# Performance work log

Hardware: AMD Instinct MI355X
Metric: run time of the kernel (lower is better)

The kernel has to match this reference:

```python
import jax, jax.numpy as jnp
import numpy as np

EPS = 1e-8  # torch.cosine_similarity norm clamp

def setup_inputs() -> dict:
    key = jax.random.key(0)
    k1, k2, k3, k4 = jax.random.split(key, 4)
    B, S, D, C = 64, 512, 768, 512
    V = jax.random.normal(k1, (B, S, D), dtype=jnp.float32)
    label_embeddings = jax.random.normal(k2, (C, D), dtype=jnp.float32)
    fc_w = jax.random.normal(k3, (C, D), dtype=jnp.float32) * 0.02
    fc_b = jax.random.normal(k4, (C,), dtype=jnp.float32) * 0.02
    return {"V": V, "label_embeddings": label_embeddings, "fc_w": fc_w, "fc_b": fc_b}

def reference(V, label_embeddings, fc_w, fc_b):
    # Normalized embeddings (cosine similarity = dot of unit vectors, norms clamped at EPS)
    Vn = V / jnp.maximum(jnp.linalg.norm(V, axis=-1, keepdims=True), EPS)
    Ln = label_embeddings / jnp.maximum(
        jnp.linalg.norm(label_embeddings, axis=-1, keepdims=True), EPS)
    # [B, S, C] cosine similarities, then max over classes -> per-token weight m [B, S]
    sims = jnp.einsum('bsd,cd->bsc', Vn, Ln)
    m = jnp.max(sims, axis=-1)
    # Softmax over sequence dim -> attention beta [B, S]
    beta = jax.nn.softmax(m, axis=-1)
    # Weighted sum of token embeddings: z = V^T beta  -> [B, D]
    z = jnp.einsum('bsd,bs->bd', V, beta)
    # Final classifier
    out = z @ fc_w.T + fc_b
    return (out, z)
```

## Files before the change

kernel.cpp:

```cpp
#include <hip/hip_runtime.h>
#include <cstdint>
#include <cstddef>

#define BB 64
#define SS 512
#define DD 768
#define CC 512

typedef __attribute__((ext_vector_type(8))) short short8;
typedef __attribute__((ext_vector_type(4))) float f32x4;

#define GLOBAL_AS __attribute__((address_space(1)))
#define LDS_AS __attribute__((address_space(3)))

static __device__ __forceinline__ unsigned short f2bf(float f) {
  union { float f; unsigned u; } v; v.f = f;
  unsigned u = v.u;
  u += 0x7FFFu + ((u >> 16) & 1u);
  return (unsigned short)(u >> 16);
}

static __device__ __forceinline__ void async_copy16(const void* g, void* l) {
  __builtin_amdgcn_global_load_lds((const GLOBAL_AS void*)g, (LDS_AS void*)l,
                                   16, 0, 0);
}

__global__ __launch_bounds__(256) void k_label_norm(const float* __restrict__ L,
                                                    unsigned short* __restrict__ Lnb) {
  const int c = blockIdx.x;
  const int tid = threadIdx.x;
  const float* row = L + (size_t)c * DD;
  float v[3];
  float s = 0.f;
#pragma unroll
  for (int k = 0; k < 3; k++) { v[k] = row[tid + 256 * k]; s += v[k] * v[k]; }
#pragma unroll
  for (int o = 32; o > 0; o >>= 1) s += __shfl_xor(s, o, 64);
  __shared__ float wsum[4];
  if ((tid & 63) == 0) wsum[tid >> 6] = s;
  __syncthreads();
  const float tot = wsum[0] + wsum[1] + wsum[2] + wsum[3];
  const float inv = 1.f / fmaxf(sqrtf(tot), 1e-8f);
  unsigned short* orow = Lnb + (size_t)c * DD;
  const int sw = c & 7;
#pragma unroll
  for (int k = 0; k < 3; k++) {
    const int d = tid + 256 * k;
    const int idx = (((d >> 3) ^ sw) << 3) | (d & 7);
    orow[idx] = f2bf(v[k] * inv);
  }
}

__global__ __launch_bounds__(256) void k_sims_max(const float* __restrict__ V,
                                                  const unsigned short* __restrict__ Lnb,
                                                  float* __restrict__ m_out) {
  const int tid = threadIdx.x;
  const int wave = tid >> 6;
  const int lane = tid & 63;
  const int q = lane >> 4;
  const int mr = lane & 15;
  const int64_t tokBase = (int64_t)blockIdx.x * 64 + wave * 16;

  __shared__ unsigned short Bs[2][16 * DD];
  __shared__ float nrmS[4][16];

  {
    const char* src = (const char*)(Lnb + (size_t)0 * 16 * DD);
    char* dst = (char*)&Bs[0][0];
#pragma unroll
    for (int i = wave; i < 24; i += 4)
      async_copy16(src + i * 1024 + lane * 16, dst + i * 1024);
  }

  const float* arow = V + (tokBase + mr) * DD + q * 8;
  short8 afrag[24];
  float nrm2 = 0.f;
#pragma unroll
  for (int kc = 0; kc < 24; kc++) {
    const float4* p = (const float4*)(arow + kc * 32);
    const float4 x = p[0];
    const float4 y = p[1];
    short8 a;
    a[0] = (short)f2bf(x.x); a[1] = (short)f2bf(x.y);
    a[2] = (short)f2bf(x.z); a[3] = (short)f2bf(x.w);
    a[4] = (short)f2bf(y.x); a[5] = (short)f2bf(y.y);
    a[6] = (short)f2bf(y.z); a[7] = (short)f2bf(y.w);
    afrag[kc] = a;
    nrm2 += x.x * x.x + x.y * x.y + x.z * x.z + x.w * x.w;
    nrm2 += y.x * y.x + y.y * y.y + y.z * y.z + y.w * y.w;
  }
  nrm2 += __shfl_xor(nrm2, 16, 64);
  nrm2 += __shfl_xor(nrm2, 32, 64);
  if (q == 0) nrmS[wave][mr] = nrm2;

  __syncthreads();

  const int sw = mr & 7;
  f32x4 vmax = {-3e38f, -3e38f, -3e38f, -3e38f};
  for (int cc = 0; cc < 32; cc++) {
    const int p = cc & 1;
    if (cc + 1 < 32) {
      const char* src = (const char*)(Lnb + (size_t)(cc + 1) * 16 * DD);
      char* dst = (char*)&Bs[p ^ 1][0];
#pragma unroll
      for (int i = wave; i < 24; i += 4)
        async_copy16(src + i * 1024 + lane * 16, dst + i * 1024);
    }
    f32x4 acc = {0.f, 0.f, 0.f, 0.f};
#pragma unroll
    for (int kc = 0; kc < 24; kc++) {
      const int off = mr * DD + (((kc << 2) + q) ^ sw) * 8;
      const short8 b = *(const short8*)&Bs[p][off];
      acc = __builtin_amdgcn_mfma_f32_16x16x32_bf16(afrag[kc], b, acc, 0, 0, 0);
    }
    vmax[0] = fmaxf(vmax[0], acc[0]);
    vmax[1] = fmaxf(vmax[1], acc[1]);
    vmax[2] = fmaxf(vmax[2], acc[2]);
    vmax[3] = fmaxf(vmax[3], acc[3]);
    __syncthreads();
  }
#pragma unroll
  for (int o = 1; o < 16; o <<= 1) {
#pragma unroll
    for (int r = 0; r < 4; r++) vmax[r] = fmaxf(vmax[r], __shfl_xor(vmax[r], o, 64));
  }
  if (mr == 0) {
#pragma unroll
    for (int r = 0; r < 4; r++) {
      const float nr = nrmS[wave][q * 4 + r];
      m_out[tokBase + q * 4 + r] = vmax[r] / fmaxf(sqrtf(nr), 1e-8f);
    }
  }
}

__global__ __launch_bounds__(256) void k_softmax(const float* __restrict__ m,
                                                 float* __restrict__ beta) {
  const int b = blockIdx.x;
  const int tid = threadIdx.x;
  const float* mb = m + (size_t)b * SS;
  const float v0 = mb[tid];
  const float v1 = mb[tid + 256];
  float mx = fmaxf(v0, v1);
#pragma unroll
  for (int o = 32; o > 0; o >>= 1) mx = fmaxf(mx, __shfl_xor(mx, o, 64));
  __shared__ float wred[4];
  if ((tid & 63) == 0) wred[tid >> 6] = mx;
  __syncthreads();
  mx = fmaxf(fmaxf(wred[0], wred[1]), fmaxf(wred[2], wred[3]));
  const float e0 = __expf(v0 - mx);
  const float e1 = __expf(v1 - mx);
  float s = e0 + e1;
#pragma unroll
  for (int o = 32; o > 0; o >>= 1) s += __shfl_xor(s, o, 64);
  __syncthreads();
  if ((tid & 63) == 0) wred[tid >> 6] = s;
  __syncthreads();
  s = wred[0] + wred[1] + wred[2] + wred[3];
  const float inv = 1.f / s;
  float* bb = beta + (size_t)b * SS;
  bb[tid] = e0 * inv;
  bb[tid + 256] = e1 * inv;
}

__global__ __launch_bounds__(192) void k_zpart(const float* __restrict__ V,
                                               const float* __restrict__ beta,
                                               float* __restrict__ zpart,
                                               int spc, int nsc) {
  const int blk = blockIdx.x;
  const int b = blk / nsc;
  const int sc = blk % nsc;
  const int tid = threadIdx.x;
  const float* vb = V + ((size_t)b * SS + (size_t)sc * spc) * DD + tid * 4;
  const float* bb = beta + (size_t)b * SS + (size_t)sc * spc;
  float4 acc = {0.f, 0.f, 0.f, 0.f};
#pragma unroll 4
  for (int s = 0; s < spc; s++) {
    const float w = bb[s];
    const float4 x = *(const float4*)(vb + (size_t)s * DD);
    acc.x += w * x.x; acc.y += w * x.y; acc.z += w * x.z; acc.w += w * x.w;
  }
  *(float4*)(zpart + (size_t)blk * DD + tid * 4) = acc;
}

__global__ __launch_bounds__(256) void k_final(const float* __restrict__ zpart,
                                               const float* __restrict__ fc_w,
                                               const float* __restrict__ fc_b,
                                               float* __restrict__ out,
                                               float* __restrict__ zout,
                                               int nsc) {
  const int b = blockIdx.x >> 1;
  const int half = blockIdx.x & 1;
  const int tid = threadIdx.x;
  __shared__ float zs[DD];
  for (int i = tid; i < DD; i += 256) {
    float s = 0.f;
    for (int sc = 0; sc < nsc; sc++) s += zpart[((size_t)b * nsc + sc) * DD + i];
    zs[i] = s;
    if (half == 0) zout[(size_t)b * DD + i] = s;
  }
  __syncthreads();
  const int c = half * 256 + tid;
  const float4* w = (const float4*)(fc_w + (size_t)c * DD);
  float acc = 0.f;
  for (int d4 = 0; d4 < DD / 4; d4++) {
    const float4 ww = w[d4];
    acc += ww.x * zs[d4 * 4] + ww.y * zs[d4 * 4 + 1] +
           ww.z * zs[d4 * 4 + 2] + ww.w * zs[d4 * 4 + 3];
  }
  out[(size_t)b * CC + c] = acc + fc_b[c];
}

extern "C" void kernel_launch(void* const* d_in, const int* in_sizes, int n_in,
                              void* d_out, int out_size, void* d_ws, size_t ws_size,
                              hipStream_t stream) {
  const float* V  = (const float*)d_in[0];
  const float* L  = (const float*)d_in[1];
  const float* fw = (const float*)d_in[2];
  const float* fb = (const float*)d_in[3];
  float* out = (float*)d_out;

  char* ws = (char*)d_ws;
  unsigned short* Lnb = (unsigned short*)ws;
  float* m     = (float*)(ws + 786432);
  float* beta  = (float*)(ws + 917504);
  float* zpart = (float*)(ws + 1048576);

  const int nsc = (ws_size >= (size_t)1048576 + 16 * BB * DD * 4) ? 16 : 8;
  const int spc = SS / nsc;

  k_label_norm<<<CC, 256, 0, stream>>>(L, Lnb);
  k_sims_max<<<512, 256, 0, stream>>>(V, Lnb, m);
  k_softmax<<<BB, 256, 0, stream>>>(m, beta);
  k_zpart<<<BB * nsc, 192, 0, stream>>>(V, beta, zpart, spc, nsc);
  k_final<<<2 * BB, 256, 0, stream>>>(zpart, fw, fb, out, out + BB * CC, nsc);
}
```

Before: 242.5 us.

## Double tokens per wave in sims kernel and fuse softmax into z partials

The sims-max kernel now runs two waves per block, each handling 32 tokens, so every LDS B-fragment load feeds two MFMAs. Each token tile also spreads its MFMAs across four independent accumulators to break the dependency chain. The separate softmax kernel is removed: each k_zpart block recomputes the row max and exp-sum from m and applies exp weights inline, saving a launch and the beta round trip at the cost of redundant reduction work per block. Register pressure rises (48 A fragments), and fewer waves per block may reduce latency hiding.

After: 259.6 us. +7.1%, slower.

```diff
diff --git a/kernel.cpp b/kernel.cpp
--- a/kernel.cpp
+++ b/kernel.cpp
@@ -51,134 +51,155 @@
   }
 }
 
-__global__ __launch_bounds__(256) void k_sims_max(const float* __restrict__ V,
-                                                  const unsigned short* __restrict__ Lnb,
-                                                  float* __restrict__ m_out) {
+__global__ __launch_bounds__(128, 1) void k_sims_max(const float* __restrict__ V,
+                                                     const unsigned short* __restrict__ Lnb,
+                                                     float* __restrict__ m_out) {
   const int tid = threadIdx.x;
   const int wave = tid >> 6;
   const int lane = tid & 63;
   const int q = lane >> 4;
   const int mr = lane & 15;
-  const int64_t tokBase = (int64_t)blockIdx.x * 64 + wave * 16;
+  const int64_t tokBase = (int64_t)blockIdx.x * 64 + wave * 32;
 
   __shared__ unsigned short Bs[2][16 * DD];
-  __shared__ float nrmS[4][16];
+  __shared__ float nrmS[2][32];
 
   {
-    const char* src = (const char*)(Lnb + (size_t)0 * 16 * DD);
+    const char* src = (const char*)Lnb;
     char* dst = (char*)&Bs[0][0];
 #pragma unroll
-    for (int i = wave; i < 24; i += 4)
+    for (int i = wave; i < 24; i += 2)
       async_copy16(src + i * 1024 + lane * 16, dst + i * 1024);
   }
 
-  const float* arow = V + (tokBase + mr) * DD + q * 8;
-  short8 afrag[24];
-  float nrm2 = 0.f;
+  const float* arow0 = V + (tokBase + mr) * DD + q * 8;
+  const float* arow1 = arow0 + 16 * DD;
+  short8 a0[24], a1[24];
+  float n0 = 0.f, n1 = 0.f;
 #pragma unroll
   for (int kc = 0; kc < 24; kc++) {
-    const float4* p = (const float4*)(arow + kc * 32);
-    const float4 x = p[0];
-    const float4 y = p[1];
+    const float4* p0 = (const float4*)(arow0 + kc * 32);
+    float4 x = p0[0];
+    float4 y = p0[1];
     short8 a;
     a[0] = (short)f2bf(x.x); a[1] = (short)f2bf(x.y);
     a[2] = (short)f2bf(x.z); a[3] = (short)f2bf(x.w);
     a[4] = (short)f2bf(y.x); a[5] = (short)f2bf(y.y);
     a[6] = (short)f2bf(y.z); a[7] = (short)f2bf(y.w);
-    afrag[kc] = a;
-    nrm2 += x.x * x.x + x.y * x.y + x.z * x.z + x.w * x.w;
-    nrm2 += y.x * y.x + y.y * y.y + y.z * y.z + y.w * y.w;
-  }
-  nrm2 += __shfl_xor(nrm2, 16, 64);
-  nrm2 += __shfl_xor(nrm2, 32, 64);
-  if (q == 0) nrmS[wave][mr] = nrm2;
+    a0[kc] = a;
+    n0 += x.x * x.x + x.y * x.y + x.z * x.z + x.w * x.w;
+    n0 += y.x * y.x + y.y * y.y + y.z * y.z + y.w * y.w;
+    const float4* p1 = (const float4*)(arow1 + kc * 32);
+    x = p1[0];
+    y = p1[1];
+    short8 c;
+    c[0] = (short)f2bf(x.x); c[1] = (short)f2bf(x.y);
+    c[2] = (short)f2bf(x.z); c[3] = (short)f2bf(x.w);
+    c[4] = (short)f2bf(y.x); c[5] = (short)f2bf(y.y);
+    c[6] = (short)f2bf(y.z); c[7] = (short)f2bf(y.w);
+    a1[kc] = c;
+    n1 += x.x * x.x + x.y * x.y + x.z * x.z + x.w * x.w;
+    n1 += y.x * y.x + y.y * y.y + y.z * y.z + y.w * y.w;
+  }
+  n0 += __shfl_xor(n0, 16, 64);
+  n0 += __shfl_xor(n0, 32, 64);
+  n1 += __shfl_xor(n1, 16, 64);
+  n1 += __shfl_xor(n1, 32, 64);
+  if (q == 0) { nrmS[wave][mr] = n0; nrmS[wave][16 + mr] = n1; }
 
   __syncthreads();
 
   const int sw = mr & 7;
-  f32x4 vmax = {-3e38f, -3e38f, -3e38f, -3e38f};
+  f32x4 vmax0 = {-3e38f, -3e38f, -3e38f, -3e38f};
+  f32x4 vmax1 = {-3e38f, -3e38f, -3e38f, -3e38f};
   for (int cc = 0; cc < 32; cc++) {
     const int p = cc & 1;
     if (cc + 1 < 32) {
       const char* src = (const char*)(Lnb + (size_t)(cc + 1) * 16 * DD);
       char* dst = (char*)&Bs[p ^ 1][0];
 #pragma unroll
-      for (int i = wave; i < 24; i += 4)
+      for (int i = wave; i < 24; i += 2)
         async_copy16(src + i * 1024 + lane * 16, dst + i * 1024);
     }
-    f32x4 acc = {0.f, 0.f, 0.f, 0.f};
+    f32x4 acc0[4], acc1[4];
+#pragma unroll
+    for (int j = 0; j < 4; j++) {
+      acc0[j] = (f32x4){0.f, 0.f, 0.f, 0.f};
+      acc1[j] = (f32x4){0.f, 0.f, 0.f, 0.f};
+    }
 #pragma unroll
     for (int kc = 0; kc < 24; kc++) {
-      const int off = mr * DD + (((kc << 2) + q) ^ sw) * 8;
+      const int off = mr * DD + ((((kc << 2) + q) ^ sw) << 3);
       const short8 b = *(const short8*)&Bs[p][off];
-      acc = __builtin_amdgcn_mfma_f32_16x16x32_bf16(afrag[kc], b, acc, 0, 0, 0);
-    }
-    vmax[0] = fmaxf(vmax[0], acc[0]);
-    vmax[1] = fmaxf(vmax[1], acc[1]);
-    vmax[2] = fmaxf(vmax[2], acc[2]);
-    vmax[3] = fmaxf(vmax[3], acc[3]);
+      acc0[kc & 3] = __builtin_amdgcn_mfma_f32_16x16x32_bf16(a0[kc], b, acc0[kc & 3], 0, 0, 0);
+      acc1[kc & 3] = __builtin_amdgcn_mfma_f32_16x16x32_bf16(a1[kc], b, acc1[kc & 3], 0, 0, 0);
+    }
+    const f32x4 s0 = (acc0[0] + acc0[1]) + (acc0[2] + acc0[3]);
+    const f32x4 s1 = (acc1[0] + acc1[1]) + (acc1[2] + acc1[3]);
+    vmax0[0] = fmaxf(vmax0[0], s0[0]); vmax0[1] = fmaxf(vmax0[1], s0[1]);
+    vmax0[2] = fmaxf(vmax0[2], s0[2]); vmax0[3] = fmaxf(vmax0[3], s0[3]);
+    vmax1[0] = fmaxf(vmax1[0], s1[0]); vmax1[1] = fmaxf(vmax1[1], s1[1]);
+    vmax1[2] = fmaxf(vmax1[2], s1[2]); vmax1[3] = fmaxf(vmax1[3], s1[3]);
     __syncthreads();
   }
 #pragma unroll
   for (int o = 1; o < 16; o <<= 1) {
 #pragma unroll
-    for (int r = 0; r < 4; r++) vmax[r] = fmaxf(vmax[r], __shfl_xor(vmax[r], o, 64));
+    for (int r = 0; r < 4; r++) {
+      vmax0[r] = fmaxf(vmax0[r], __shfl_xor(vmax0[r], o, 64));
+      vmax1[r] = fmaxf(vmax1[r], __shfl_xor(vmax1[r], o, 64));
+    }
   }
   if (mr == 0) {
 #pragma unroll
     for (int r = 0; r < 4; r++) {
-      const float nr = nrmS[wave][q * 4 + r];
-      m_out[tokBase + q * 4 + r] = vmax[r] / fmaxf(sqrtf(nr), 1e-8f);
-    }
-  }
-}
-
-__global__ __launch_bounds__(256) void k_softmax(const float* __restrict__ m,
-                                                 float* __restrict__ beta) {
-  const int b = blockIdx.x;
-  const int tid = threadIdx.x;
-  const float* mb = m + (size_t)b * SS;
-  const float v0 = mb[tid];
-  const float v1 = mb[tid + 256];
-  float mx = fmaxf(v0, v1);
-#pragma unroll
-  for (int o = 32; o > 0; o >>= 1) mx = fmaxf(mx, __shfl_xor(mx, o, 64));
-  __shared__ float wred[4];
-  if ((tid & 63) == 0) wred[tid >> 6] = mx;
-  __syncthreads();
-  mx = fmaxf(fmaxf(wred[0], wred[1]), fmaxf(wred[2], wred[3]));
-  const float e0 = __expf(v0 - mx);
-  const float e1 = __expf(v1 - mx);
-  float s = e0 + e1;
-#pragma unroll
-  for (int o = 32; o > 0; o >>= 1) s += __shfl_xor(s, o, 64);
-  __syncthreads();
-  if ((tid & 63) == 0) wred[tid >> 6] = s;
-  __syncthreads();
-  s = wred[0] + wred[1] + wred[2] + wred[3];
-  const float inv = 1.f / s;
-  float* bb = beta + (size_t)b * SS;
-  bb[tid] = e0 * inv;
-  bb[tid + 256] = e1 * inv;
+      const float d0 = nrmS[wave][q * 4 + r];
+      const float d1 = nrmS[wave][16 + q * 4 + r];
+      m_out[tokBase + q * 4 + r] = vmax0[r] / fmaxf(sqrtf(d0), 1e-8f);
+      m_out[tokBase + 16 + q * 4 + r] = vmax1[r] / fmaxf(sqrtf(d1), 1e-8f);
+    }
+  }
 }
 
 __global__ __launch_bounds__(192) void k_zpart(const float* __restrict__ V,
-                                               const float* __restrict__ beta,
+                                               const float* __restrict__ m,
                                                float* __restrict__ zpart,
                                                int spc, int nsc) {
   const int blk = blockIdx.x;
   const int b = blk / nsc;
   const int sc = blk % nsc;
   const int tid = threadIdx.x;
+  const float* mb = m + (size_t)b * SS;
+
+  const float x0 = mb[tid];
+  const float x1 = mb[tid + 192];
+  const float x2 = (tid < 128) ? mb[tid + 384] : -3e38f;
+  float mx = fmaxf(fmaxf(x0, x1), x2);
+#pragma unroll
+  for (int o = 32; o > 0; o >>= 1) mx = fmaxf(mx, __shfl_xor(mx, o, 64));
+  __shared__ float redm[3];
+  __shared__ float reds[3];
+  if ((tid & 63) == 0) redm[tid >> 6] = mx;
+  __syncthreads();
+  mx = fmaxf(redm[0], fmaxf(redm[1], redm[2]));
+  float es = __expf(x0 - mx) + __expf(x1 - mx) +
+             ((tid < 128) ? __expf(x2 - mx) : 0.f);
+#pragma unroll
+  for (int o = 32; o > 0; o >>= 1) es += __shfl_xor(es, o, 64);
+  if ((tid & 63) == 0) reds[tid >> 6] = es;
+  __syncthreads();
+  const float inv = 1.f / (reds[0] + reds[1] + reds[2]);
+
   const float* vb = V + ((size_t)b * SS + (size_t)sc * spc) * DD + tid * 4;
-  const float* bb = beta + (size_t)b * SS + (size_t)sc * spc;
+  const float* msc = mb + (size_t)sc * spc;
   float4 acc = {0.f, 0.f, 0.f, 0.f};
 #pragma unroll 4
   for (int s = 0; s < spc; s++) {
-    const float w = bb[s];
+    const float w = __expf(msc[s] - mx);
     const float4 x = *(const float4*)(vb + (size_t)s * DD);
     acc.x += w * x.x; acc.y += w * x.y; acc.z += w * x.z; acc.w += w * x.w;
   }
+  acc.x *= inv; acc.y *= inv; acc.z *= inv; acc.w *= inv;
   *(float4*)(zpart + (size_t)blk * DD + tid * 4) = acc;
 }
 
@@ -222,15 +243,13 @@
   char* ws = (char*)d_ws;
   unsigned short* Lnb = (unsigned short*)ws;
   float* m     = (float*)(ws + 786432);
-  float* beta  = (float*)(ws + 917504);
-  float* zpart = (float*)(ws + 1048576);
-
-  const int nsc = (ws_size >= (size_t)1048576 + 16 * BB * DD * 4) ? 16 : 8;
+  float* zpart = (float*)(ws + 917504);
+
+  const int nsc = (ws_size >= (size_t)917504 + (size_t)16 * BB * DD * 4) ? 16 : 8;
   const int spc = SS / nsc;
 
   k_label_norm<<<CC, 256, 0, stream>>>(L, Lnb);
-  k_sims_max<<<512, 256, 0, stream>>>(V, Lnb, m);
-  k_softmax<<<BB, 256, 0, stream>>>(m, beta);
-  k_zpart<<<BB * nsc, 192, 0, stream>>>(V, beta, zpart, spc, nsc);
+  k_sims_max<<<512, 128, 0, stream>>>(V, Lnb, m);
+  k_zpart<<<BB * nsc, 192, 0, stream>>>(V, m, zpart, spc, nsc);
   k_final<<<2 * BB, 256, 0, stream>>>(zpart, fw, fb, out, out + BB * CC, nsc);
 }
```

## Fuse softmax into weighted-sum kernel and split MFMA accumulator chains

Applied to the files above, without the earlier changes.

Removes the separate softmax kernel: each zpart block recomputes the per-batch max and exp-sum over 512 m values, then weights its slice with unnormalized exps and scales by the inverse sum at the end. This saves a kernel launch and the beta round trip, at the cost of redundant reductions in every block. The V loads in the weighted sum are batched eight at a time for more memory-level parallelism. In the sims kernel, the 24-step MFMA chain is split across four independent accumulators to break the serial dependence.

After: 269.1 us. 1.11x slower.

```diff
diff --git a/kernel.cpp b/kernel.cpp
--- a/kernel.cpp
+++ b/kernel.cpp
@@ -65,7 +65,7 @@
   __shared__ float nrmS[4][16];
 
   {
-    const char* src = (const char*)(Lnb + (size_t)0 * 16 * DD);
+    const char* src = (const char*)Lnb;
     char* dst = (char*)&Bs[0][0];
 #pragma unroll
     for (int i = wave; i < 24; i += 4)
@@ -106,17 +106,20 @@
       for (int i = wave; i < 24; i += 4)
         async_copy16(src + i * 1024 + lane * 16, dst + i * 1024);
     }
-    f32x4 acc = {0.f, 0.f, 0.f, 0.f};
+    f32x4 acc[4];
+#pragma unroll
+    for (int j = 0; j < 4; j++) acc[j] = (f32x4){0.f, 0.f, 0.f, 0.f};
 #pragma unroll
     for (int kc = 0; kc < 24; kc++) {
-      const int off = mr * DD + (((kc << 2) + q) ^ sw) * 8;
+      const int off = mr * DD + ((((kc << 2) + q) ^ sw) << 3);
       const short8 b = *(const short8*)&Bs[p][off];
-      acc = __builtin_amdgcn_mfma_f32_16x16x32_bf16(afrag[kc], b, acc, 0, 0, 0);
-    }
-    vmax[0] = fmaxf(vmax[0], acc[0]);
-    vmax[1] = fmaxf(vmax[1], acc[1]);
-    vmax[2] = fmaxf(vmax[2], acc[2]);
-    vmax[3] = fmaxf(vmax[3], acc[3]);
+      acc[kc & 3] = __builtin_amdgcn_mfma_f32_16x16x32_bf16(afrag[kc], b, acc[kc & 3], 0, 0, 0);
+    }
+    const f32x4 s = (acc[0] + acc[1]) + (acc[2] + acc[3]);
+    vmax[0] = fmaxf(vmax[0], s[0]);
+    vmax[1] = fmaxf(vmax[1], s[1]);
+    vmax[2] = fmaxf(vmax[2], s[2]);
+    vmax[3] = fmaxf(vmax[3], s[3]);
     __syncthreads();
   }
 #pragma unroll
@@ -133,52 +136,52 @@
   }
 }
 
-__global__ __launch_bounds__(256) void k_softmax(const float* __restrict__ m,
-                                                 float* __restrict__ beta) {
-  const int b = blockIdx.x;
-  const int tid = threadIdx.x;
-  const float* mb = m + (size_t)b * SS;
-  const float v0 = mb[tid];
-  const float v1 = mb[tid + 256];
-  float mx = fmaxf(v0, v1);
-#pragma unroll
-  for (int o = 32; o > 0; o >>= 1) mx = fmaxf(mx, __shfl_xor(mx, o, 64));
-  __shared__ float wred[4];
-  if ((tid & 63) == 0) wred[tid >> 6] = mx;
-  __syncthreads();
-  mx = fmaxf(fmaxf(wred[0], wred[1]), fmaxf(wred[2], wred[3]));
-  const float e0 = __expf(v0 - mx);
-  const float e1 = __expf(v1 - mx);
-  float s = e0 + e1;
-#pragma unroll
-  for (int o = 32; o > 0; o >>= 1) s += __shfl_xor(s, o, 64);
-  __syncthreads();
-  if ((tid & 63) == 0) wred[tid >> 6] = s;
-  __syncthreads();
-  s = wred[0] + wred[1] + wred[2] + wred[3];
-  const float inv = 1.f / s;
-  float* bb = beta + (size_t)b * SS;
-  bb[tid] = e0 * inv;
-  bb[tid + 256] = e1 * inv;
-}
-
 __global__ __launch_bounds__(192) void k_zpart(const float* __restrict__ V,
-                                               const float* __restrict__ beta,
+                                               const float* __restrict__ m,
                                                float* __restrict__ zpart,
                                                int spc, int nsc) {
   const int blk = blockIdx.x;
   const int b = blk / nsc;
   const int sc = blk % nsc;
   const int tid = threadIdx.x;
+  const float* mb = m + (size_t)b * SS;
+
+  const float x0 = mb[tid];
+  const float x1 = mb[tid + 192];
+  const float x2 = (tid < 128) ? mb[tid + 384] : -3e38f;
+  float mx = fmaxf(fmaxf(x0, x1), x2);
+#pragma unroll
+  for (int o = 32; o > 0; o >>= 1) mx = fmaxf(mx, __shfl_xor(mx, o, 64));
+  __shared__ float redm[3];
+  __shared__ float reds[3];
+  __shared__ float wl[64];
+  if ((tid & 63) == 0) redm[tid >> 6] = mx;
+  __syncthreads();
+  mx = fmaxf(redm[0], fmaxf(redm[1], redm[2]));
+  float es = __expf(x0 - mx) + __expf(x1 - mx) +
+             ((tid < 128) ? __expf(x2 - mx) : 0.f);
+#pragma unroll
+  for (int o = 32; o > 0; o >>= 1) es += __shfl_xor(es, o, 64);
+  if ((tid & 63) == 0) reds[tid >> 6] = es;
+  if (tid < spc) wl[tid] = __expf(mb[sc * spc + tid] - mx);
+  __syncthreads();
+  const float inv = 1.f / (reds[0] + reds[1] + reds[2]);
+
   const float* vb = V + ((size_t)b * SS + (size_t)sc * spc) * DD + tid * 4;
-  const float* bb = beta + (size_t)b * SS + (size_t)sc * spc;
   float4 acc = {0.f, 0.f, 0.f, 0.f};
-#pragma unroll 4
-  for (int s = 0; s < spc; s++) {
-    const float w = bb[s];
-    const float4 x = *(const float4*)(vb + (size_t)s * DD);
-    acc.x += w * x.x; acc.y += w * x.y; acc.z += w * x.z; acc.w += w * x.w;
-  }
+  for (int s0 = 0; s0 < spc; s0 += 8) {
+    float4 v[8];
+#pragma unroll
+    for (int j = 0; j < 8; j++)
+      v[j] = *(const float4*)(vb + (size_t)(s0 + j) * DD);
+#pragma unroll
+    for (int j = 0; j < 8; j++) {
+      const float w = wl[s0 + j];
+      acc.x += w * v[j].x; acc.y += w * v[j].y;
+      acc.z += w * v[j].z; acc.w += w * v[j].w;
+    }
+  }
+  acc.x *= inv; acc.y *= inv; acc.z *= inv; acc.w *= inv;
   *(float4*)(zpart + (size_t)blk * DD + tid * 4) = acc;
 }
 
@@ -222,15 +225,13 @@
   char* ws = (char*)d_ws;
   unsigned short* Lnb = (unsigned short*)ws;
   float* m     = (float*)(ws + 786432);
-  float* beta  = (float*)(ws + 917504);
-  float* zpart = (float*)(ws + 1048576);
-
-  const int nsc = (ws_size >= (size_t)1048576 + 16 * BB * DD * 4) ? 16 : 8;
+  float* zpart = (float*)(ws + 917504);
+
+  const int nsc = (ws_size >= (size_t)917504 + (size_t)16 * BB * DD * 4) ? 16 : 8;
   const int spc = SS / nsc;
 
   k_label_norm<<<CC, 256, 0, stream>>>(L, Lnb);
   k_sims_max<<<512, 256, 0, stream>>>(V, Lnb, m);
-  k_softmax<<<BB, 256, 0, stream>>>(m, beta);
-  k_zpart<<<BB * nsc, 192, 0, stream>>>(V, beta, zpart, spc, nsc);
+  k_zpart<<<BB * nsc, 192, 0, stream>>>(V, m, zpart, spc, nsc);
   k_final<<<2 * BB, 256, 0, stream>>>(zpart, fw, fb, out, out + BB * CC, nsc);
 }
```
